# Optimization experiments

Hardware: AMD Instinct MI355X
Metric: run time of the kernel (lower is better)

Reference implementation:

```python
import jax, jax.numpy as jnp
import numpy as np

# Each of the 16 soft binary logic ops is a polynomial c0 + c1*a + c2*b + c3*a*b.
# Rows below are the [c0, c1, c2, c3] coefficients for ops 0..15 (same math as bin_op).
_OP_COEF = np.array([
    [0., 0., 0., 0.],   # 0: zeros
    [0., 0., 0., 1.],   # 1: a*b
    [0., 1., 0., -1.],  # 2: a - a*b
    [0., 1., 0., 0.],   # 3: a
    [0., 0., 1., -1.],  # 4: b - a*b
    [0., 0., 1., 0.],   # 5: b
    [0., 1., 1., -2.],  # 6: a + b - 2ab
    [0., 1., 1., -1.],  # 7: a + b - ab
    [1., -1., -1., 1.], # 8: 1 - (a + b - ab)
    [1., -1., -1., 2.], # 9: 1 - (a + b - 2ab)
    [1., 0., -1., 0.],  # 10: 1 - b
    [1., 0., -1., 1.],  # 11: 1 - b + ab
    [1., -1., 0., 0.],  # 12: 1 - a
    [1., -1., 0., 1.],  # 13: 1 - a + ab
    [1., 0., 0., -1.],  # 14: 1 - a*b
    [1., 0., 0., 0.],   # 15: ones
], dtype=np.float32)

K_CLASSES = 10
TAU = 30.0


def logic_layer(x, w, idx_a, idx_b):
    # x: [B, in_dim], w: [out_dim, 16], idx_a/idx_b: [out_dim]
    probs = jax.nn.softmax(w, axis=-1)                 # [O, 16]
    coef = probs @ jnp.asarray(_OP_COEF)               # [O, 4]
    a = x[:, idx_a]                                    # [B, O]
    b = x[:, idx_b]                                    # [B, O]
    # weighted mixture of 16 ops == polynomial in (1, a, b, a*b)
    return coef[:, 0] + coef[:, 1] * a + coef[:, 2] * b + coef[:, 3] * (a * b)


def group_sum(x, k, tau):
    B = x.shape[0]
    return x.reshape(B, k, x.shape[-1] // k).sum(-1) / tau


def setup_inputs() -> dict:
    key = jax.random.key(0)
    ks = jax.random.split(key, 10)
    B, D0, D1, D2, D3 = 4096, 1024, 8192, 8192, 10240
    return {
        "x": jax.random.uniform(ks[0], (B, D0), dtype=jnp.float32),
        "w1": jax.random.normal(ks[1], (D1, 16), dtype=jnp.float32),
        "w2": jax.random.normal(ks[2], (D2, 16), dtype=jnp.float32),
        "w3": jax.random.normal(ks[3], (D3, 16), dtype=jnp.float32),
        "idx_a1": jax.random.randint(ks[4], (D1,), 0, D0, dtype=jnp.int32),
        "idx_b1": jax.random.randint(ks[5], (D1,), 0, D0, dtype=jnp.int32),
        "idx_a2": jax.random.randint(ks[6], (D2,), 0, D1, dtype=jnp.int32),
        "idx_b2": jax.random.randint(ks[7], (D2,), 0, D1, dtype=jnp.int32),
        "idx_a3": jax.random.randint(ks[8], (D3,), 0, D2, dtype=jnp.int32),
        "idx_b3": jax.random.randint(ks[9], (D3,), 0, D2, dtype=jnp.int32),
    }


def reference(x, w1, w2, w3, idx_a1, idx_b1, idx_a2, idx_b2, idx_a3, idx_b3):
    h = logic_layer(x, w1, idx_a1, idx_b1)
    h = logic_layer(h, w2, idx_a2, idx_b2)
    h = logic_layer(h, w3, idx_a3, idx_b3)
    return group_sum(h, K_CLASSES, TAU)   # [B, 10]
```

## Files before the change

### kernel.cpp

```cpp
#include <hip/hip_runtime.h>
#include <hip/hip_fp16.h>
#include <stdint.h>

#define D0 1024
#define D1 8192
#define D2 8192
#define D3 10240
#define B_ROWS 4096

#define SM_XB     0
#define SM_H2     8192
#define SM_CSUM   (8192 + 65536)
#define SM_BYTES  (8192 + 65536 + 160)

__device__ __forceinline__ float4 softmax_coef(const float* __restrict__ w) {
    const float4* wv = (const float4*)w;
    float4 q0 = wv[0], q1 = wv[1], q2 = wv[2], q3 = wv[3];
    float wa[16] = {q0.x, q0.y, q0.z, q0.w, q1.x, q1.y, q1.z, q1.w,
                    q2.x, q2.y, q2.z, q2.w, q3.x, q3.y, q3.z, q3.w};
    float m = wa[0];
#pragma unroll
    for (int i = 1; i < 16; ++i) m = fmaxf(m, wa[i]);
    float e[16], s = 0.f;
#pragma unroll
    for (int i = 0; i < 16; ++i) { e[i] = __expf(wa[i] - m); s += e[i]; }
    float inv = 1.f / s;
    static constexpr float OPC[16][4] = {
        {0.f, 0.f, 0.f, 0.f}, {0.f, 0.f, 0.f, 1.f}, {0.f, 1.f, 0.f, -1.f}, {0.f, 1.f, 0.f, 0.f},
        {0.f, 0.f, 1.f, -1.f}, {0.f, 0.f, 1.f, 0.f}, {0.f, 1.f, 1.f, -2.f}, {0.f, 1.f, 1.f, -1.f},
        {1.f, -1.f, -1.f, 1.f}, {1.f, -1.f, -1.f, 2.f}, {1.f, 0.f, -1.f, 0.f}, {1.f, 0.f, -1.f, 1.f},
        {1.f, -1.f, 0.f, 0.f}, {1.f, -1.f, 0.f, 1.f}, {1.f, 0.f, 0.f, -1.f}, {1.f, 0.f, 0.f, 0.f}};
    float c0 = 0.f, c1 = 0.f, c2 = 0.f, c3 = 0.f;
#pragma unroll
    for (int i = 0; i < 16; ++i) {
        float p = e[i] * inv;
        c0 += p * OPC[i][0];
        c1 += p * OPC[i][1];
        c2 += p * OPC[i][2];
        c3 += p * OPC[i][3];
    }
    return make_float4(c0, c1, c2, c3);
}

__device__ __forceinline__ uint2 pack_coef(float4 c) {
    uint2 r;
    r.x = __builtin_bit_cast(uint32_t, __floats2half2_rn(c.x, c.y));
    r.y = __builtin_bit_cast(uint32_t, __floats2half2_rn(c.z, c.w));
    return r;
}

__global__ __launch_bounds__(64) void prep_kernel(
    const float* __restrict__ w1, const float* __restrict__ w2,
    const float* __restrict__ w3,
    const int* __restrict__ ia1, const int* __restrict__ ib1,
    const int* __restrict__ ia2, const int* __restrict__ ib2,
    const int* __restrict__ ia3, const int* __restrict__ ib3,
    uint4* __restrict__ bcM1, uint4* __restrict__ bcM2,
    uint4* __restrict__ d3M) {
    int G = blockIdx.x * 64 + threadIdx.x;
    if (G < D2) {
        int g = G;
        int pa = ia2[g], pb = ib2[g];
        float4 cO = softmax_coef(w2 + (size_t)g * 16);
        float4 cA = softmax_coef(w1 + (size_t)pa * 16);
        float4 cB = softmax_coef(w1 + (size_t)pb * 16);
        uint32_t xiA = (uint32_t)(ia1[pa] << 3) | ((uint32_t)(ib1[pa] << 3) << 16);
        uint32_t xiB = (uint32_t)(ia1[pb] << 3) | ((uint32_t)(ib1[pb] << 3) << 16);
        uint2 o = pack_coef(cO), a = pack_coef(cA), b = pack_coef(cB);
        bcM1[g] = make_uint4(xiA, xiB, o.x, o.y);
        bcM2[g] = make_uint4(a.x, a.y, b.x, b.y);
    } else {
        int g = G - D2;
        float4 cO = softmax_coef(w3 + (size_t)g * 16);
        uint2 o = pack_coef(cO);
        uint32_t xi = (uint32_t)(ia3[g] << 3) | ((uint32_t)(ib3[g] << 3) << 16);
        d3M[g] = make_uint4(xi, o.x, o.y, 0u);
    }
}

__device__ __forceinline__ uint2 gate4(uint2 av, uint2 bv, uint2 cf) {
    __half2 p = __builtin_bit_cast(__half2, cf.x);
    __half2 q = __builtin_bit_cast(__half2, cf.y);
    __half2 c0 = __low2half2(p), c1 = __high2half2(p);
    __half2 c2 = __low2half2(q), c3 = __high2half2(q);
    __half2 a01 = __builtin_bit_cast(__half2, av.x);
    __half2 a23 = __builtin_bit_cast(__half2, av.y);
    __half2 b01 = __builtin_bit_cast(__half2, bv.x);
    __half2 b23 = __builtin_bit_cast(__half2, bv.y);
    __half2 h01 = __hfma2(a01, __hfma2(b01, c3, c1), __hfma2(b01, c2, c0));
    __half2 h23 = __hfma2(a23, __hfma2(b23, c3, c1), __hfma2(b23, c2, c0));
    uint2 r;
    r.x = __builtin_bit_cast(uint32_t, h01);
    r.y = __builtin_bit_cast(uint32_t, h23);
    return r;
}

__global__ __launch_bounds__(1024, 8) void fused_kernel(
    const float* __restrict__ x, const uint4* __restrict__ bcM1,
    const uint4* __restrict__ bcM2, const uint4* __restrict__ d3M,
    float* __restrict__ out) {
    extern __shared__ char sm[];
    uint2* xb = (uint2*)(sm + SM_XB);
    float* csum = (float*)(sm + SM_CSUM);

    const int t = threadIdx.x;
    const int rowbase = blockIdx.x << 2;
    const int tg = t << 1;

    uint4 m1a_n = bcM1[tg];
    uint4 m1b_n = bcM1[tg + 1];

    {
        const float* xp = x + (size_t)rowbase * D0 + t;
        float v0 = xp[0];
        float v1 = xp[D0];
        float v2 = xp[2 * D0];
        float v3 = xp[3 * D0];
        uint2 v;
        v.x = __builtin_bit_cast(uint32_t, __floats2half2_rn(v0, v1));
        v.y = __builtin_bit_cast(uint32_t, __floats2half2_rn(v2, v3));
        xb[t] = v;
    }
    if (t < 40) csum[t] = 0.f;
    __syncthreads();

#pragma unroll
    for (int k = 0; k < 4; ++k) {
        uint4 m1a = m1a_n, m1b = m1b_n;
        int g = tg + (k << 11);
        uint4 m2a = bcM2[g];
        uint4 m2b = bcM2[g + 1];
        if (k < 3) {
            int gn = tg + ((k + 1) << 11);
            m1a_n = bcM1[gn];
            m1b_n = bcM1[gn + 1];
        }
        uint2 aa0 = *(const uint2*)(sm + (m1a.x & 0xffffu));
        uint2 ab0 = *(const uint2*)(sm + (m1a.x >> 16));
        uint2 ba0 = *(const uint2*)(sm + (m1a.y & 0xffffu));
        uint2 bb0 = *(const uint2*)(sm + (m1a.y >> 16));
        uint2 aa1 = *(const uint2*)(sm + (m1b.x & 0xffffu));
        uint2 ab1 = *(const uint2*)(sm + (m1b.x >> 16));
        uint2 ba1 = *(const uint2*)(sm + (m1b.y & 0xffffu));
        uint2 bb1 = *(const uint2*)(sm + (m1b.y >> 16));
        uint2 h0 = gate4(gate4(aa0, ab0, make_uint2(m2a.x, m2a.y)),
                         gate4(ba0, bb0, make_uint2(m2a.z, m2a.w)),
                         make_uint2(m1a.z, m1a.w));
        uint2 h1v = gate4(gate4(aa1, ab1, make_uint2(m2b.x, m2b.y)),
                          gate4(ba1, bb1, make_uint2(m2b.z, m2b.w)),
                          make_uint2(m1b.z, m1b.w));
        ((uint4*)(sm + SM_H2))[(k << 10) + t] = make_uint4(h0.x, h0.y, h1v.x, h1v.y);
    }
    __syncthreads();

    {
        const int wv = t >> 6, lane = t & 63;
        const int gbase = wv * 640;
        const int cA = gbase >> 10;
        const int bnd = (cA + 1) << 10;
        float s0[4] = {0.f, 0.f, 0.f, 0.f};
        float s1[4] = {0.f, 0.f, 0.f, 0.f};
#pragma unroll
        for (int j = 0; j < 5; ++j) {
            int gc = gbase + (j << 7);
            int g = gc + (lane << 1);
            uint4 ma = d3M[g];
            uint4 mb = d3M[g + 1];
            uint2 av0 = *(const uint2*)(sm + SM_H2 + (ma.x & 0xffffu));
            uint2 bv0 = *(const uint2*)(sm + SM_H2 + (ma.x >> 16));
            uint2 av1 = *(const uint2*)(sm + SM_H2 + (mb.x & 0xffffu));
            uint2 bv1 = *(const uint2*)(sm + SM_H2 + (mb.x >> 16));
            uint2 h0 = gate4(av0, bv0, make_uint2(ma.y, ma.z));
            uint2 h1v = gate4(av1, bv1, make_uint2(mb.y, mb.z));
            __half2 p01 = __hadd2(__builtin_bit_cast(__half2, h0.x),
                                  __builtin_bit_cast(__half2, h1v.x));
            __half2 p23 = __hadd2(__builtin_bit_cast(__half2, h0.y),
                                  __builtin_bit_cast(__half2, h1v.y));
            float f0 = __low2float(p01), f1 = __high2float(p01);
            float f2 = __low2float(p23), f3 = __high2float(p23);
            if (gc < bnd) {
                s0[0] += f0; s0[1] += f1; s0[2] += f2; s0[3] += f3;
            } else {
                s1[0] += f0; s1[1] += f1; s1[2] += f2; s1[3] += f3;
            }
        }
#pragma unroll
        for (int m = 1; m < 64; m <<= 1) {
#pragma unroll
            for (int r = 0; r < 4; ++r) {
                s0[r] += __shfl_xor(s0[r], m, 64);
                s1[r] += __shfl_xor(s1[r], m, 64);
            }
        }
        if (lane == 0) {
#pragma unroll
            for (int r = 0; r < 4; ++r) atomicAdd(&csum[cA * 4 + r], s0[r]);
            if (gbase + 640 > bnd) {
#pragma unroll
                for (int r = 0; r < 4; ++r) atomicAdd(&csum[(cA + 1) * 4 + r], s1[r]);
            }
        }
    }
    __syncthreads();

    if (t < 40) {
        int c = t >> 2, r = t & 3;
        out[(size_t)(rowbase + r) * 10 + c] = csum[t] * (1.0f / 30.0f);
    }
}

extern "C" void kernel_launch(void* const* d_in, const int* in_sizes, int n_in,
                              void* d_out, int out_size, void* d_ws, size_t ws_size,
                              hipStream_t stream) {
    const float* x = (const float*)d_in[0];
    const float* w1 = (const float*)d_in[1];
    const float* w2 = (const float*)d_in[2];
    const float* w3 = (const float*)d_in[3];
    const int* ia1 = (const int*)d_in[4];
    const int* ib1 = (const int*)d_in[5];
    const int* ia2 = (const int*)d_in[6];
    const int* ib2 = (const int*)d_in[7];
    const int* ia3 = (const int*)d_in[8];
    const int* ib3 = (const int*)d_in[9];
    float* out = (float*)d_out;

    char* p = (char*)d_ws;
    uint4* bcM1 = (uint4*)p;    p += (size_t)D2 * 16;
    uint4* bcM2 = (uint4*)p;    p += (size_t)D2 * 16;
    uint4* d3M = (uint4*)p;

    hipFuncSetAttribute(reinterpret_cast<const void*>(fused_kernel),
                        hipFuncAttributeMaxDynamicSharedMemorySize, SM_BYTES);

    prep_kernel<<<(D2 + D3) / 64, 64, 0, stream>>>(
        w1, w2, w3, ia1, ib1, ia2, ib2, ia3, ib3, bcM1, bcM2, d3M);
    fused_kernel<<<B_ROWS / 4, 1024, SM_BYTES, stream>>>(x, bcM1, bcM2, d3M, out);
}
```

Measured before the change: 106.9 us.

## Process eight batch rows per block to amortize gate metadata loads

```diff
diff --git a/kernel.cpp b/kernel.cpp
--- a/kernel.cpp
+++ b/kernel.cpp
@@ -9,9 +9,9 @@
 #define B_ROWS 4096
 
 #define SM_XB     0
-#define SM_H2     8192
-#define SM_CSUM   (8192 + 65536)
-#define SM_BYTES  (8192 + 65536 + 160)
+#define SM_H2     16384
+#define SM_CSUM   (16384 + 131072)
+#define SM_BYTES  (16384 + 131072 + 320)
 
 __device__ __forceinline__ float4 softmax_coef(const float* __restrict__ w) {
     const float4* wv = (const float4*)w;
@@ -64,8 +64,8 @@
         float4 cO = softmax_coef(w2 + (size_t)g * 16);
         float4 cA = softmax_coef(w1 + (size_t)pa * 16);
         float4 cB = softmax_coef(w1 + (size_t)pb * 16);
-        uint32_t xiA = (uint32_t)(ia1[pa] << 3) | ((uint32_t)(ib1[pa] << 3) << 16);
-        uint32_t xiB = (uint32_t)(ia1[pb] << 3) | ((uint32_t)(ib1[pb] << 3) << 16);
+        uint32_t xiA = (uint32_t)(ia1[pa] << 4) | ((uint32_t)(ib1[pa] << 4) << 16);
+        uint32_t xiB = (uint32_t)(ia1[pb] << 4) | ((uint32_t)(ib1[pb] << 4) << 16);
         uint2 o = pack_coef(cO), a = pack_coef(cA), b = pack_coef(cB);
         bcM1[g] = make_uint4(xiA, xiB, o.x, o.y);
         bcM2[g] = make_uint4(a.x, a.y, b.x, b.y);
@@ -73,38 +73,37 @@
         int g = G - D2;
         float4 cO = softmax_coef(w3 + (size_t)g * 16);
         uint2 o = pack_coef(cO);
-        uint32_t xi = (uint32_t)(ia3[g] << 3) | ((uint32_t)(ib3[g] << 3) << 16);
-        d3M[g] = make_uint4(xi, o.x, o.y, 0u);
-    }
-}
-
-__device__ __forceinline__ uint2 gate4(uint2 av, uint2 bv, uint2 cf) {
+        uint32_t ei = (uint32_t)ia3[g] | ((uint32_t)ib3[g] << 16);
+        d3M[g] = make_uint4(ei, o.x, o.y, 0u);
+    }
+}
+
+__device__ __forceinline__ uint4 gate8(uint4 av, uint4 bv, uint2 cf) {
     __half2 p = __builtin_bit_cast(__half2, cf.x);
     __half2 q = __builtin_bit_cast(__half2, cf.y);
     __half2 c0 = __low2half2(p), c1 = __high2half2(p);
     __half2 c2 = __low2half2(q), c3 = __high2half2(q);
-    __half2 a01 = __builtin_bit_cast(__half2, av.x);
-    __half2 a23 = __builtin_bit_cast(__half2, av.y);
-    __half2 b01 = __builtin_bit_cast(__half2, bv.x);
-    __half2 b23 = __builtin_bit_cast(__half2, bv.y);
-    __half2 h01 = __hfma2(a01, __hfma2(b01, c3, c1), __hfma2(b01, c2, c0));
-    __half2 h23 = __hfma2(a23, __hfma2(b23, c3, c1), __hfma2(b23, c2, c0));
-    uint2 r;
-    r.x = __builtin_bit_cast(uint32_t, h01);
-    r.y = __builtin_bit_cast(uint32_t, h23);
+    uint4 r;
+#pragma unroll
+    for (int i = 0; i < 4; ++i) {
+        __half2 a = __builtin_bit_cast(__half2, (&av.x)[i]);
+        __half2 b = __builtin_bit_cast(__half2, (&bv.x)[i]);
+        __half2 h = __hfma2(a, __hfma2(b, c3, c1), __hfma2(b, c2, c0));
+        (&r.x)[i] = __builtin_bit_cast(uint32_t, h);
+    }
     return r;
 }
 
-__global__ __launch_bounds__(1024, 8) void fused_kernel(
+__global__ __launch_bounds__(1024, 4) void fused_kernel(
     const float* __restrict__ x, const uint4* __restrict__ bcM1,
     const uint4* __restrict__ bcM2, const uint4* __restrict__ d3M,
     float* __restrict__ out) {
     extern __shared__ char sm[];
-    uint2* xb = (uint2*)(sm + SM_XB);
+    uint4* xb = (uint4*)(sm + SM_XB);
     float* csum = (float*)(sm + SM_CSUM);
 
     const int t = threadIdx.x;
-    const int rowbase = blockIdx.x << 2;
+    const int rowbase = blockIdx.x << 3;
     const int tg = t << 1;
 
     uint4 m1a_n = bcM1[tg];
@@ -112,16 +111,16 @@
 
     {
         const float* xp = x + (size_t)rowbase * D0 + t;
-        float v0 = xp[0];
-        float v1 = xp[D0];
-        float v2 = xp[2 * D0];
-        float v3 = xp[3 * D0];
-        uint2 v;
-        v.x = __builtin_bit_cast(uint32_t, __floats2half2_rn(v0, v1));
-        v.y = __builtin_bit_cast(uint32_t, __floats2half2_rn(v2, v3));
+        uint4 v;
+#pragma unroll
+        for (int i = 0; i < 4; ++i) {
+            float va = xp[(size_t)(2 * i) * D0];
+            float vb = xp[(size_t)(2 * i + 1) * D0];
+            (&v.x)[i] = __builtin_bit_cast(uint32_t, __floats2half2_rn(va, vb));
+        }
         xb[t] = v;
     }
-    if (t < 40) csum[t] = 0.f;
+    if (t < 80) csum[t] = 0.f;
     __syncthreads();
 
 #pragma unroll
@@ -135,21 +134,22 @@
             m1a_n = bcM1[gn];
             m1b_n = bcM1[gn + 1];
         }
-        uint2 aa0 = *(const uint2*)(sm + (m1a.x & 0xffffu));
-        uint2 ab0 = *(const uint2*)(sm + (m1a.x >> 16));
-        uint2 ba0 = *(const uint2*)(sm + (m1a.y & 0xffffu));
-        uint2 bb0 = *(const uint2*)(sm + (m1a.y >> 16));
-        uint2 aa1 = *(const uint2*)(sm + (m1b.x & 0xffffu));
-        uint2 ab1 = *(const uint2*)(sm + (m1b.x >> 16));
-        uint2 ba1 = *(const uint2*)(sm + (m1b.y & 0xffffu));
-        uint2 bb1 = *(const uint2*)(sm + (m1b.y >> 16));
-        uint2 h0 = gate4(gate4(aa0, ab0, make_uint2(m2a.x, m2a.y)),
-                         gate4(ba0, bb0, make_uint2(m2a.z, m2a.w)),
+        uint4 aa0 = *(const uint4*)(sm + (m1a.x & 0xffffu));
+        uint4 ab0 = *(const uint4*)(sm + (m1a.x >> 16));
+        uint4 ba0 = *(const uint4*)(sm + (m1a.y & 0xffffu));
+        uint4 bb0 = *(const uint4*)(sm + (m1a.y >> 16));
+        uint4 aa1 = *(const uint4*)(sm + (m1b.x & 0xffffu));
+        uint4 ab1 = *(const uint4*)(sm + (m1b.x >> 16));
+        uint4 ba1 = *(const uint4*)(sm + (m1b.y & 0xffffu));
+        uint4 bb1 = *(const uint4*)(sm + (m1b.y >> 16));
+        uint4 h0 = gate8(gate8(aa0, ab0, make_uint2(m2a.x, m2a.y)),
+                         gate8(ba0, bb0, make_uint2(m2a.z, m2a.w)),
                          make_uint2(m1a.z, m1a.w));
-        uint2 h1v = gate4(gate4(aa1, ab1, make_uint2(m2b.x, m2b.y)),
-                          gate4(ba1, bb1, make_uint2(m2b.z, m2b.w)),
+        uint4 h1v = gate8(gate8(aa1, ab1, make_uint2(m2b.x, m2b.y)),
+                          gate8(ba1, bb1, make_uint2(m2b.z, m2b.w)),
                           make_uint2(m1b.z, m1b.w));
-        ((uint4*)(sm + SM_H2))[(k << 10) + t] = make_uint4(h0.x, h0.y, h1v.x, h1v.y);
+        *(uint4*)(sm + SM_H2 + ((uint32_t)g << 4)) = h0;
+        *(uint4*)(sm + SM_H2 + ((uint32_t)(g + 1) << 4)) = h1v;
     }
     __syncthreads();
 
@@ -158,53 +158,50 @@
         const int gbase = wv * 640;
         const int cA = gbase >> 10;
         const int bnd = (cA + 1) << 10;
-        float s0[4] = {0.f, 0.f, 0.f, 0.f};
-        float s1[4] = {0.f, 0.f, 0.f, 0.f};
+        float s0[8] = {0.f, 0.f, 0.f, 0.f, 0.f, 0.f, 0.f, 0.f};
+        float s1[8] = {0.f, 0.f, 0.f, 0.f, 0.f, 0.f, 0.f, 0.f};
 #pragma unroll
         for (int j = 0; j < 5; ++j) {
             int gc = gbase + (j << 7);
             int g = gc + (lane << 1);
             uint4 ma = d3M[g];
             uint4 mb = d3M[g + 1];
-            uint2 av0 = *(const uint2*)(sm + SM_H2 + (ma.x & 0xffffu));
-            uint2 bv0 = *(const uint2*)(sm + SM_H2 + (ma.x >> 16));
-            uint2 av1 = *(const uint2*)(sm + SM_H2 + (mb.x & 0xffffu));
-            uint2 bv1 = *(const uint2*)(sm + SM_H2 + (mb.x >> 16));
-            uint2 h0 = gate4(av0, bv0, make_uint2(ma.y, ma.z));
-            uint2 h1v = gate4(av1, bv1, make_uint2(mb.y, mb.z));
-            __half2 p01 = __hadd2(__builtin_bit_cast(__half2, h0.x),
-                                  __builtin_bit_cast(__half2, h1v.x));
-            __half2 p23 = __hadd2(__builtin_bit_cast(__half2, h0.y),
-                                  __builtin_bit_cast(__half2, h1v.y));
-            float f0 = __low2float(p01), f1 = __high2float(p01);
-            float f2 = __low2float(p23), f3 = __high2float(p23);
-            if (gc < bnd) {
-                s0[0] += f0; s0[1] += f1; s0[2] += f2; s0[3] += f3;
-            } else {
-                s1[0] += f0; s1[1] += f1; s1[2] += f2; s1[3] += f3;
+            uint4 av0 = *(const uint4*)(sm + SM_H2 + ((ma.x & 0xffffu) << 4));
+            uint4 bv0 = *(const uint4*)(sm + SM_H2 + ((ma.x >> 16) << 4));
+            uint4 av1 = *(const uint4*)(sm + SM_H2 + ((mb.x & 0xffffu) << 4));
+            uint4 bv1 = *(const uint4*)(sm + SM_H2 + ((mb.x >> 16) << 4));
+            uint4 h0 = gate8(av0, bv0, make_uint2(ma.y, ma.z));
+            uint4 h1v = gate8(av1, bv1, make_uint2(mb.y, mb.z));
+            float* s = (gc < bnd) ? s0 : s1;
+#pragma unroll
+            for (int i = 0; i < 4; ++i) {
+                __half2 pr = __hadd2(__builtin_bit_cast(__half2, (&h0.x)[i]),
+                                     __builtin_bit_cast(__half2, (&h1v.x)[i]));
+                s[2 * i] += __low2float(pr);
+                s[2 * i + 1] += __high2float(pr);
             }
         }
 #pragma unroll
         for (int m = 1; m < 64; m <<= 1) {
 #pragma unroll
-            for (int r = 0; r < 4; ++r) {
+            for (int r = 0; r < 8; ++r) {
                 s0[r] += __shfl_xor(s0[r], m, 64);
                 s1[r] += __shfl_xor(s1[r], m, 64);
             }
         }
         if (lane == 0) {
 #pragma unroll
-            for (int r = 0; r < 4; ++r) atomicAdd(&csum[cA * 4 + r], s0[r]);
+            for (int r = 0; r < 8; ++r) atomicAdd(&csum[cA * 8 + r], s0[r]);
             if (gbase + 640 > bnd) {
 #pragma unroll
-                for (int r = 0; r < 4; ++r) atomicAdd(&csum[(cA + 1) * 4 + r], s1[r]);
+                for (int r = 0; r < 8; ++r) atomicAdd(&csum[(cA + 1) * 8 + r], s1[r]);
             }
         }
     }
     __syncthreads();
 
-    if (t < 40) {
-        int c = t >> 2, r = t & 3;
+    if (t < 80) {
+        int c = t >> 3, r = t & 7;
         out[(size_t)(rowbase + r) * 10 + c] = csum[t] * (1.0f / 30.0f);
     }
 }
@@ -234,5 +231,5 @@
 
     prep_kernel<<<(D2 + D3) / 64, 64, 0, stream>>>(
         w1, w2, w3, ia1, ib1, ia2, ib2, ia3, ib3, bcM1, bcM2, d3M);
-    fused_kernel<<<B_ROWS / 4, 1024, SM_BYTES, stream>>>(x, bcM1, bcM2, d3M, out);
-}
+    fused_kernel<<<B_ROWS / 8, 1024, SM_BYTES, stream>>>(x, bcM1, bcM2, d3M, out);
+}
```

Measured after the change: 105.4 us, median of 2. No clear change (-1.4%).
